# Kernel tuning notes

Measured on AMD Instinct MI355X. Metric: run time of the kernel, lower is better.

The kernel has to match this reference:

```python
import jax, jax.numpy as jnp
import numpy as np

NEG_INF = -1e9  # matches masked_fill value -1000000000.0
LEAKY_SLOPE = 0.2


def setup_inputs() -> dict:
    key = jax.random.key(0)
    k1, k2, k3, k4 = jax.random.split(key, 4)
    B, N, D_in, D_out = 8, 2048, 256, 256
    x = jax.random.normal(k1, (B, N, D_in), dtype=jnp.float32)
    adj_matrix = jax.random.randint(k2, (B, N, N), 0, 2, dtype=jnp.int32)
    # torch nn.Linear weights: W is [out, in], attention a is [1, 2*out]
    W = jax.random.normal(k3, (D_out, D_in), dtype=jnp.float32) / np.sqrt(D_in)
    a = jax.random.normal(k4, (1, 2 * D_out), dtype=jnp.float32) / np.sqrt(2 * D_out)
    return {"x": x, "adj_matrix": adj_matrix, "W": W, "a": a}


def reference(x, adj_matrix, W, a):
    # h = W(x): [B, N, D_out]
    h = jnp.einsum('bnd,od->bno', x, W)
    D = h.shape[-1]
    # attention(concat(h_i, h_j)) == h_i @ a_left + h_j @ a_right (bias-free linear)
    a_left, a_right = a[0, :D], a[0, D:]
    e = (h @ a_left)[:, :, None] + (h @ a_right)[:, None, :]  # [B, N, N]
    e = jnp.where(e > 0, e, LEAKY_SLOPE * e)  # LeakyReLU(0.2)
    e = jnp.where(adj_matrix == 0, NEG_INF, e)
    alpha = jax.nn.softmax(e, axis=-1)
    return jnp.einsum('bij,bjd->bid', alpha, h)
```

## Files before the change

### kernel.cpp

```cpp
#include <hip/hip_runtime.h>
#include <hip/hip_bf16.h>

typedef __attribute__((ext_vector_type(8))) __bf16 bf16x8;
typedef __attribute__((ext_vector_type(4))) float f32x4;
typedef __attribute__((ext_vector_type(4))) int int4v;

#define NB 8
#define NN 2048
#define ND 256
#define L2E 1.44269504f
#define AS1 __attribute__((address_space(1)))
#define AS3 __attribute__((address_space(3)))

__global__ __launch_bounds__(256) void k2_elr(
    const float* __restrict__ x, const float* __restrict__ W,
    const float* __restrict__ a, float* __restrict__ elc,
    float* __restrict__ erx) {
  __shared__ float wls[ND], wrs[ND];
  int t = threadIdx.x;
  {
    float swl = 0.f, swr = 0.f;
    for (int o = 0; o < ND; ++o) {
      float wv = W[(long)o * ND + t];
      swl = fmaf(a[o], wv, swl);
      swr = fmaf(a[ND + o], wv, swr);
    }
    wls[t] = swl;
    wrs[t] = swr;
  }
  __syncthreads();
  int r = t >> 2, q = t & 3;
  long row = (long)blockIdx.x * 64 + r;
  const f32x4* xr = (const f32x4*)(x + row * ND);
  float sl = 0.f, sr = 0.f;
#pragma unroll
  for (int ii = 0; ii < 16; ++ii) {
    int idx = q + (ii << 2);
    f32x4 xv = xr[idx];
    f32x4 lv = *(const f32x4*)(wls + idx * 4);
    f32x4 rv = *(const f32x4*)(wrs + idx * 4);
    sl += xv[0] * lv[0] + xv[1] * lv[1] + xv[2] * lv[2] + xv[3] * lv[3];
    sr += xv[0] * rv[0] + xv[1] * rv[1] + xv[2] * rv[2] + xv[3] * rv[3];
  }
  sl += __shfl_xor(sl, 1);
  sl += __shfl_xor(sl, 2);
  sr += __shfl_xor(sr, 1);
  sr += __shfl_xor(sr, 2);
  if (q == 0) {
    elc[row] = (-0.8f * sl - 16.0f) * L2E;
    erx[row] = (sr - 16.0f) * L2E;
  }
}

__global__ __launch_bounds__(256) void k1_h(
    const float* __restrict__ x, const float* __restrict__ W,
    __bf16* __restrict__ hT2) {
  __shared__ __bf16 hlds[256 * 34];
  int tid = threadIdx.x;
  int wid = tid >> 6, lane = tid & 63;
  int msub = wid & 1, nh = wid >> 1;
  int lrow = lane & 15, kg = lane >> 4;
  int m0 = blockIdx.x * 32;
  int row = m0 + msub * 16 + lrow;

  f32x4 acc[8];
#pragma unroll
  for (int f = 0; f < 8; ++f) acc[f] = (f32x4){0.f, 0.f, 0.f, 0.f};

#pragma unroll
  for (int k0 = 0; k0 < ND; k0 += 32) {
    int kk = k0 + kg * 8;
    const f32x4* xa = (const f32x4*)(x + (long)row * ND + kk);
    f32x4 a0 = xa[0], a1 = xa[1];
    bf16x8 afrag;
    afrag[0] = (__bf16)a0[0]; afrag[1] = (__bf16)a0[1];
    afrag[2] = (__bf16)a0[2]; afrag[3] = (__bf16)a0[3];
    afrag[4] = (__bf16)a1[0]; afrag[5] = (__bf16)a1[1];
    afrag[6] = (__bf16)a1[2]; afrag[7] = (__bf16)a1[3];
#pragma unroll
    for (int f = 0; f < 8; ++f) {
      int o = nh * 128 + f * 16 + lrow;
      const f32x4* wb = (const f32x4*)(W + (long)o * ND + kk);
      f32x4 b0 = wb[0], b1 = wb[1];
      bf16x8 bfrag;
      bfrag[0] = (__bf16)b0[0]; bfrag[1] = (__bf16)b0[1];
      bfrag[2] = (__bf16)b0[2]; bfrag[3] = (__bf16)b0[3];
      bfrag[4] = (__bf16)b1[0]; bfrag[5] = (__bf16)b1[1];
      bfrag[6] = (__bf16)b1[2]; bfrag[7] = (__bf16)b1[3];
      acc[f] = __builtin_amdgcn_mfma_f32_16x16x32_bf16(afrag, bfrag, acc[f], 0, 0, 0);
    }
  }

#pragma unroll
  for (int f = 0; f < 8; ++f) {
    int d = nh * 128 + f * 16 + lrow;
#pragma unroll
    for (int r = 0; r < 4; ++r) {
      int nloc = msub * 16 + kg * 4 + r;
      hlds[d * 34 + nloc] = (__bf16)acc[f][r];
    }
  }
  __syncthreads();
  {
    int b = m0 >> 11;
    int jc = (m0 & (NN - 1)) >> 5;
    const int* src = (const int*)(hlds + tid * 34);
    int tmp[16];
#pragma unroll
    for (int j = 0; j < 16; ++j) tmp[j] = src[j];
    __bf16* dst = hT2 + (((long)b * 64 + jc) * 256 + tid) * 32;
#pragma unroll
    for (int j = 0; j < 4; ++j)
      *(int4v*)(dst + j * 8) = *(int4v*)(tmp + j * 4);
  }
}

__global__ __launch_bounds__(256, 2) void k3_main(
    const int* __restrict__ adj, const __bf16* __restrict__ hT2,
    const float* __restrict__ elc, const float* __restrict__ erx,
    float* __restrict__ out) {
  __shared__ __bf16 hbuf[4][8192];
  __shared__ float er_lds[NN];
  __shared__ unsigned mask_lds[2048];

  int blk = blockIdx.x;
  int b = blk & 7;
  int it = blk >> 3;
  int tid = threadIdx.x;
  int wid = tid >> 6, lane = tid & 63;
  int lrow = lane & 15, kg = lane >> 4;
  int kg8 = kg * 8;

  const __bf16* hT2b = hT2 + (long)b * 64 * 8192;
  const int* adjb = adj + ((long)b * NN + (long)it * 32) * NN;
  const int* adjw = adjb + (long)wid * 8 * NN;
  const float* erxb = erx + (long)b * NN;

  float c1s0 = elc[b * NN + it * 32 + lrow];
  float c1s1 = elc[b * NN + it * 32 + 16 + lrow];

  __builtin_amdgcn_global_load_lds((const AS1 void*)(erxb + tid * 4),
                                   (AS3 void*)(er_lds + tid * 4), 16, 0, 0);
  __builtin_amdgcn_global_load_lds((const AS1 void*)(erxb + 1024 + tid * 4),
                                   (AS3 void*)(er_lds + 1024 + tid * 4), 16, 0, 0);

  int d0 = tid >> 2, slot = tid & 3;
  int jlog = slot ^ ((tid >> 3) & 3);
  const __bf16* sgbase = hT2b + d0 * 32 + jlog * 8;

  int hoff = (wid * 64 + lrow) * 64 + (kg ^ ((lrow >> 1) & 3)) * 16;

  f32x4 acc[2][4];
#pragma unroll
  for (int g = 0; g < 2; ++g)
#pragma unroll
    for (int f = 0; f < 4; ++f) acc[g][f] = (f32x4){0.f, 0.f, 0.f, 0.f};
  float den0 = 0.f, den1 = 0.f;

  int av0[4], av1[4];

#define STAGEH(BI, TCV)                                                       \
  {                                                                           \
    const __bf16* s_ = sgbase + (long)(TCV)*8192;                             \
    _Pragma("unroll") for (int rr = 0; rr < 4; ++rr) {                        \
      __builtin_amdgcn_global_load_lds(                                       \
          (const AS1 void*)(s_ + rr * 2048),                                  \
          (AS3 void*)(&hbuf[BI][(rr * 256 + tid) * 8]), 16, 0, 0);            \
    }                                                                         \
  }

#define ADJLOAD(S, P, H)                                                      \
  {                                                                           \
    const int* ap_ = adjw + (long)(H)*4 * NN + (long)(P)*64 + lane;           \
    _Pragma("unroll") for (int i = 0; i < 4; ++i)                             \
        av##S[i] = ap_[(long)i * NN];                                         \
  }

#define BALLOT(S, P, H)                                                       \
  {                                                                           \
    _Pragma("unroll") for (int i = 0; i < 4; ++i) {                           \
      unsigned long long mb_ = __ballot(av##S[i] != 0);                       \
      int R_ = wid * 8 + (H)*4 + i;                                           \
      if (lane == 0) {                                                        \
        mask_lds[R_ * 64 + ((2 * (P)) ^ (R_ & 31))] = (unsigned)mb_;          \
        mask_lds[R_ * 64 + ((2 * (P) + 1) ^ (R_ & 31))] = (unsigned)(mb_ >> 32); \
      }                                                                       \
    }                                                                         \
  }

#define COMPUTE(BI, TCV)                                                      \
  {                                                                           \
    unsigned msh0 = mask_lds[lrow * 64 + ((TCV) ^ lrow)] >> kg8;              \
    unsigned msh1 = mask_lds[(lrow + 16) * 64 + ((TCV) ^ lrow ^ 16)] >> kg8;  \
    const float* ep_ = er_lds + (TCV)*32 + kg8;                               \
    f32x4 x16a = *(const f32x4*)(ep_);                                        \
    f32x4 x16b = *(const f32x4*)(ep_ + 4);                                    \
    bf16x8 pf0, pf1;                                                          \
    float ps0 = 0.f, ps1 = 0.f;                                               \
    _Pragma("unroll") for (int e = 0; e < 8; ++e) {                           \
      float x16 = (e < 4) ? x16a[e] : x16b[e - 4];                            \
      float x02 = fmaf(0.2f, x16, 4.61662413f);                               \
      float m0_ = fmaxf(x16, x02 + c1s0);                                     \
      float m1_ = fmaxf(x16, x02 + c1s1);                                     \
      float p0 = __builtin_amdgcn_exp2f(m0_);                                 \
      float p1 = __builtin_amdgcn_exp2f(m1_);                                 \
      p0 = ((msh0 >> e) & 1u) ? p0 : 0.0f;                                    \
      p1 = ((msh1 >> e) & 1u) ? p1 : 0.0f;                                    \
      ps0 += p0; ps1 += p1;                                                   \
      pf0[e] = (__bf16)p0; pf1[e] = (__bf16)p1;                               \
    }                                                                         \
    den0 += ps0; den1 += ps1;                                                 \
    const char* hb_ = (const char*)&hbuf[BI][0];                              \
    __builtin_amdgcn_s_setprio(1);                                            \
    _Pragma("unroll") for (int f = 0; f < 4; ++f) {                           \
      bf16x8 bfr = *(const bf16x8*)(hb_ + hoff + f * 1024);                   \
      acc[0][f] = __builtin_amdgcn_mfma_f32_16x16x32_bf16(pf0, bfr, acc[0][f], 0, 0, 0); \
      acc[1][f] = __builtin_amdgcn_mfma_f32_16x16x32_bf16(pf1, bfr, acc[1][f], 0, 0, 0); \
    }                                                                         \
    __builtin_amdgcn_s_setprio(0);                                            \
  }

#define WAITX(VMN)                                                        \
  asm volatile("s_waitcnt vmcnt(" VMN ") lgkmcnt(0)" ::: "memory");       \
  __builtin_amdgcn_s_barrier();

  STAGEH(0, 0);
  STAGEH(1, 1);
  ADJLOAD(0, 0, 0);
  ADJLOAD(1, 0, 1);
  asm volatile("s_waitcnt vmcnt(0)" ::: "memory");
  BALLOT(0, 0, 0);
  BALLOT(1, 0, 1);
  ADJLOAD(0, 1, 0);
  ADJLOAD(1, 1, 1);
  asm volatile("s_waitcnt lgkmcnt(0)" ::: "memory");
  __builtin_amdgcn_s_barrier();

  for (int T = 0; T < 15; ++T) {
    int tc = T * 4;
    WAITX("8"); STAGEH(2, tc + 2); BALLOT(0, (tc >> 1) + 1, 0);
    ADJLOAD(0, (tc >> 1) + 2, 0); COMPUTE(0, tc);
    WAITX("8"); STAGEH(3, tc + 3); BALLOT(1, (tc >> 1) + 1, 1);
    ADJLOAD(1, (tc >> 1) + 2, 1); COMPUTE(1, tc + 1);
    WAITX("8"); STAGEH(0, tc + 4); BALLOT(0, (tc >> 1) + 2, 0);
    ADJLOAD(0, (tc >> 1) + 3, 0); COMPUTE(2, tc + 2);
    WAITX("8"); STAGEH(1, tc + 5); BALLOT(1, (tc >> 1) + 2, 1);
    ADJLOAD(1, (tc >> 1) + 3, 1); COMPUTE(3, tc + 3);
  }
  WAITX("8"); STAGEH(2, 62); BALLOT(0, 31, 0); COMPUTE(0, 60);
  WAITX("4"); STAGEH(3, 63); BALLOT(1, 31, 1); COMPUTE(1, 61);
  WAITX("4"); COMPUTE(2, 62);
  WAITX("0"); COMPUTE(3, 63);

#undef STAGEH
#undef ADJLOAD
#undef BALLOT
#undef COMPUTE
#undef WAITX

  den0 += __shfl_xor(den0, 16);
  den0 += __shfl_xor(den0, 32);
  den1 += __shfl_xor(den1, 16);
  den1 += __shfl_xor(den1, 32);
  float rdiv0[4], rdiv1[4];
#pragma unroll
  for (int r = 0; r < 4; ++r) {
    rdiv0[r] = 1.0f / __shfl(den0, kg * 4 + r);
    rdiv1[r] = 1.0f / __shfl(den1, kg * 4 + r);
  }

  float* outb = out + ((long)b * NN + (long)it * 32) * ND;
#pragma unroll
  for (int f = 0; f < 4; ++f) {
    int dcol = wid * 64 + f * 16 + lrow;
#pragma unroll
    for (int r = 0; r < 4; ++r) {
      int rr = kg * 4 + r;
      outb[(long)rr * ND + dcol] = acc[0][f][r] * rdiv0[r];
      outb[(long)(16 + rr) * ND + dcol] = acc[1][f][r] * rdiv1[r];
    }
  }
}

extern "C" void kernel_launch(void* const* d_in, const int* in_sizes, int n_in,
                              void* d_out, int out_size, void* d_ws,
                              size_t ws_size, hipStream_t stream) {
  const float* x = (const float*)d_in[0];
  const int* adj = (const int*)d_in[1];
  const float* W = (const float*)d_in[2];
  const float* a = (const float*)d_in[3];
  float* out = (float*)d_out;

  char* ws = (char*)d_ws;
  const size_t base = 8u * 1024u * 1024u;
  __bf16* hT2 = (__bf16*)ws;
  float* elc = (float*)(ws + base);
  float* erx = (float*)(ws + base + 65536u);

  k1_h<<<dim3(512), dim3(256), 0, stream>>>(x, W, hT2);
  k2_elr<<<dim3(256), dim3(256), 0, stream>>>(x, W, a, elc, erx);
  k3_main<<<dim3(512), dim3(256), 0, stream>>>(adj, hT2, elc, erx, out);
}
```

Measured before the change: 125.5 us.

## Split waves over j-halves and D-halves, read adjacency directly per lane

Re-partitions the main attention kernel so each wave owns half the key columns (alternating 32-column chunks) and half the output features, with 128-wide accumulators per wave. The ballot-based bitmask path through LDS is dropped: each lane loads its own adjacency ints as int4 vectors and uses them directly as the mask. The staged h buffer becomes double-buffered 64-key stages with a full vmcnt(0) wait each step. Partial results from the two j-halves are combined through LDS at the end. This removes ballot and LDS mask traffic but doubles accumulator registers and weakens prefetch depth.

```diff
diff --git a/kernel.cpp b/kernel.cpp
--- a/kernel.cpp
+++ b/kernel.cpp
@@ -119,23 +119,22 @@
     const int* __restrict__ adj, const __bf16* __restrict__ hT2,
     const float* __restrict__ elc, const float* __restrict__ erx,
     float* __restrict__ out) {
-  __shared__ __bf16 hbuf[4][8192];
+  __shared__ __bf16 hbuf[2][4][4096];
   __shared__ float er_lds[NN];
-  __shared__ unsigned mask_lds[2048];
+  __shared__ float denb[4][32];
 
   int blk = blockIdx.x;
   int b = blk & 7;
   int it = blk >> 3;
   int tid = threadIdx.x;
   int wid = tid >> 6, lane = tid & 63;
-  int lrow = lane & 15, kg = lane >> 4;
-  int kg8 = kg * 8;
+  int jw = wid >> 1, dw = wid & 1;
+  int lrow = lane & 15, kg = lane >> 4, kg8 = kg * 8;
 
   const __bf16* hT2b = hT2 + (long)b * 64 * 8192;
-  const int* adjb = adj + ((long)b * NN + (long)it * 32) * NN;
-  const int* adjw = adjb + (long)wid * 8 * NN;
+  const int* adjr0 = adj + ((long)b * NN + it * 32 + lrow) * NN;
+  const int* adjr1 = adjr0 + 16 * NN;
   const float* erxb = erx + (long)b * NN;
-
   float c1s0 = elc[b * NN + it * 32 + lrow];
   float c1s1 = elc[b * NN + it * 32 + 16 + lrow];
 
@@ -144,141 +143,132 @@
   __builtin_amdgcn_global_load_lds((const AS1 void*)(erxb + 1024 + tid * 4),
                                    (AS3 void*)(er_lds + 1024 + tid * 4), 16, 0, 0);
 
-  int d0 = tid >> 2, slot = tid & 3;
-  int jlog = slot ^ ((tid >> 3) & 3);
-  const __bf16* sgbase = hT2b + d0 * 32 + jlog * 8;
-
-  int hoff = (wid * 64 + lrow) * 64 + (kg ^ ((lrow >> 1) & 3)) * 16;
-
-  f32x4 acc[2][4];
-#pragma unroll
-  for (int g = 0; g < 2; ++g)
-#pragma unroll
-    for (int f = 0; f < 4; ++f) acc[g][f] = (f32x4){0.f, 0.f, 0.f, 0.f};
+  int jlog = (tid & 3) ^ ((tid >> 3) & 3);
+  int stoff = (tid >> 2) * 32 + jlog * 8;
+  int hoff = lrow * 64 + (kg ^ ((lrow >> 1) & 3)) * 16;
+
+  f32x4 acc0[8], acc1[8];
+#pragma unroll
+  for (int f = 0; f < 8; ++f) {
+    acc0[f] = (f32x4){0.f, 0.f, 0.f, 0.f};
+    acc1[f] = (f32x4){0.f, 0.f, 0.f, 0.f};
+  }
   float den0 = 0.f, den1 = 0.f;
-
-  int av0[4], av1[4];
-
-#define STAGEH(BI, TCV)                                                       \
+  int4v av0_0, av0_1, av0_2, av0_3, av1_0, av1_1, av1_2, av1_3;
+
+#define STAGE(PH, SP)                                                         \
   {                                                                           \
-    const __bf16* s_ = sgbase + (long)(TCV)*8192;                             \
-    _Pragma("unroll") for (int rr = 0; rr < 4; ++rr) {                        \
+    long cb_ = (long)(2 * (SP)) * 8192;                                       \
+    _Pragma("unroll") for (int s = 0; s < 8; ++s) {                           \
+      const __bf16* src_ = hT2b + cb_ + (s >> 2) * 8192 + ((s >> 1) & 1) * 4096 \
+                           + (s & 1) * 2048 + stoff;                          \
       __builtin_amdgcn_global_load_lds(                                       \
-          (const AS1 void*)(s_ + rr * 2048),                                  \
-          (AS3 void*)(&hbuf[BI][(rr * 256 + tid) * 8]), 16, 0, 0);            \
+          (const AS1 void*)src_,                                              \
+          (AS3 void*)(&hbuf[PH][s >> 1][(s & 1) * 2048 + tid * 8]), 16, 0, 0); \
     }                                                                         \
   }
 
-#define ADJLOAD(S, P, H)                                                      \
+#define ADJL(SET, SP)                                                         \
   {                                                                           \
-    const int* ap_ = adjw + (long)(H)*4 * NN + (long)(P)*64 + lane;           \
-    _Pragma("unroll") for (int i = 0; i < 4; ++i)                             \
-        av##S[i] = ap_[(long)i * NN];                                         \
-  }
-
-#define BALLOT(S, P, H)                                                       \
+    const int* a0_ = adjr0 + (long)(2 * (SP) + jw) * 32 + kg8;                \
+    const int* a1_ = adjr1 + (long)(2 * (SP) + jw) * 32 + kg8;                \
+    av##SET##_0 = *(const int4v*)a0_;                                         \
+    av##SET##_1 = *(const int4v*)(a0_ + 4);                                   \
+    av##SET##_2 = *(const int4v*)a1_;                                         \
+    av##SET##_3 = *(const int4v*)(a1_ + 4);                                   \
+  }
+
+#define COMP(PH, SET, SP)                                                     \
   {                                                                           \
-    _Pragma("unroll") for (int i = 0; i < 4; ++i) {                           \
-      unsigned long long mb_ = __ballot(av##S[i] != 0);                       \
-      int R_ = wid * 8 + (H)*4 + i;                                           \
-      if (lane == 0) {                                                        \
-        mask_lds[R_ * 64 + ((2 * (P)) ^ (R_ & 31))] = (unsigned)mb_;          \
-        mask_lds[R_ * 64 + ((2 * (P) + 1) ^ (R_ & 31))] = (unsigned)(mb_ >> 32); \
-      }                                                                       \
-    }                                                                         \
-  }
-
-#define COMPUTE(BI, TCV)                                                      \
-  {                                                                           \
-    unsigned msh0 = mask_lds[lrow * 64 + ((TCV) ^ lrow)] >> kg8;              \
-    unsigned msh1 = mask_lds[(lrow + 16) * 64 + ((TCV) ^ lrow ^ 16)] >> kg8;  \
-    const float* ep_ = er_lds + (TCV)*32 + kg8;                               \
-    f32x4 x16a = *(const f32x4*)(ep_);                                        \
-    f32x4 x16b = *(const f32x4*)(ep_ + 4);                                    \
+    const float* ep_ = er_lds + (2 * (SP) + jw) * 32 + kg8;                   \
+    f32x4 xa_ = *(const f32x4*)ep_;                                           \
+    f32x4 xb_ = *(const f32x4*)(ep_ + 4);                                     \
     bf16x8 pf0, pf1;                                                          \
     float ps0 = 0.f, ps1 = 0.f;                                               \
     _Pragma("unroll") for (int e = 0; e < 8; ++e) {                           \
-      float x16 = (e < 4) ? x16a[e] : x16b[e - 4];                            \
+      float x16 = (e < 4) ? xa_[e] : xb_[e - 4];                              \
       float x02 = fmaf(0.2f, x16, 4.61662413f);                               \
+      int a0v = (e < 4) ? av##SET##_0[e] : av##SET##_1[e - 4];                \
+      int a1v = (e < 4) ? av##SET##_2[e] : av##SET##_3[e - 4];                \
       float m0_ = fmaxf(x16, x02 + c1s0);                                     \
       float m1_ = fmaxf(x16, x02 + c1s1);                                     \
       float p0 = __builtin_amdgcn_exp2f(m0_);                                 \
       float p1 = __builtin_amdgcn_exp2f(m1_);                                 \
-      p0 = ((msh0 >> e) & 1u) ? p0 : 0.0f;                                    \
-      p1 = ((msh1 >> e) & 1u) ? p1 : 0.0f;                                    \
+      p0 = a0v ? p0 : 0.0f;                                                   \
+      p1 = a1v ? p1 : 0.0f;                                                   \
       ps0 += p0; ps1 += p1;                                                   \
       pf0[e] = (__bf16)p0; pf1[e] = (__bf16)p1;                               \
     }                                                                         \
     den0 += ps0; den1 += ps1;                                                 \
-    const char* hb_ = (const char*)&hbuf[BI][0];                              \
+    const char* hb_ = (const char*)&hbuf[PH][wid][0];                         \
     __builtin_amdgcn_s_setprio(1);                                            \
-    _Pragma("unroll") for (int f = 0; f < 4; ++f) {                           \
+    _Pragma("unroll") for (int f = 0; f < 8; ++f) {                           \
       bf16x8 bfr = *(const bf16x8*)(hb_ + hoff + f * 1024);                   \
-      acc[0][f] = __builtin_amdgcn_mfma_f32_16x16x32_bf16(pf0, bfr, acc[0][f], 0, 0, 0); \
-      acc[1][f] = __builtin_amdgcn_mfma_f32_16x16x32_bf16(pf1, bfr, acc[1][f], 0, 0, 0); \
+      acc0[f] = __builtin_amdgcn_mfma_f32_16x16x32_bf16(pf0, bfr, acc0[f], 0, 0, 0); \
+      acc1[f] = __builtin_amdgcn_mfma_f32_16x16x32_bf16(pf1, bfr, acc1[f], 0, 0, 0); \
     }                                                                         \
     __builtin_amdgcn_s_setprio(0);                                            \
   }
 
-#define WAITX(VMN)                                                        \
-  asm volatile("s_waitcnt vmcnt(" VMN ") lgkmcnt(0)" ::: "memory");       \
+#define WAIT0                                         \
+  asm volatile("s_waitcnt vmcnt(0)" ::: "memory");    \
   __builtin_amdgcn_s_barrier();
 
-  STAGEH(0, 0);
-  STAGEH(1, 1);
-  ADJLOAD(0, 0, 0);
-  ADJLOAD(1, 0, 1);
-  asm volatile("s_waitcnt vmcnt(0)" ::: "memory");
-  BALLOT(0, 0, 0);
-  BALLOT(1, 0, 1);
-  ADJLOAD(0, 1, 0);
-  ADJLOAD(1, 1, 1);
-  asm volatile("s_waitcnt lgkmcnt(0)" ::: "memory");
-  __builtin_amdgcn_s_barrier();
+  ADJL(0, 0);
+  STAGE(0, 0);
 
   for (int T = 0; T < 15; ++T) {
-    int tc = T * 4;
-    WAITX("8"); STAGEH(2, tc + 2); BALLOT(0, (tc >> 1) + 1, 0);
-    ADJLOAD(0, (tc >> 1) + 2, 0); COMPUTE(0, tc);
-    WAITX("8"); STAGEH(3, tc + 3); BALLOT(1, (tc >> 1) + 1, 1);
-    ADJLOAD(1, (tc >> 1) + 2, 1); COMPUTE(1, tc + 1);
-    WAITX("8"); STAGEH(0, tc + 4); BALLOT(0, (tc >> 1) + 2, 0);
-    ADJLOAD(0, (tc >> 1) + 3, 0); COMPUTE(2, tc + 2);
-    WAITX("8"); STAGEH(1, tc + 5); BALLOT(1, (tc >> 1) + 2, 1);
-    ADJLOAD(1, (tc >> 1) + 3, 1); COMPUTE(3, tc + 3);
-  }
-  WAITX("8"); STAGEH(2, 62); BALLOT(0, 31, 0); COMPUTE(0, 60);
-  WAITX("4"); STAGEH(3, 63); BALLOT(1, 31, 1); COMPUTE(1, 61);
-  WAITX("4"); COMPUTE(2, 62);
-  WAITX("0"); COMPUTE(3, 63);
-
-#undef STAGEH
-#undef ADJLOAD
-#undef BALLOT
-#undef COMPUTE
-#undef WAITX
+    int ke = 2 * T;
+    WAIT0; ADJL(1, ke + 1); STAGE(1, ke + 1); COMP(0, 0, ke);
+    WAIT0; ADJL(0, ke + 2); STAGE(0, ke + 2); COMP(1, 1, ke + 1);
+  }
+  WAIT0; ADJL(1, 31); STAGE(1, 31); COMP(0, 0, 30);
+  WAIT0; COMP(1, 1, 31);
+
+#undef STAGE
+#undef ADJL
+#undef COMP
+#undef WAIT0
 
   den0 += __shfl_xor(den0, 16);
   den0 += __shfl_xor(den0, 32);
   den1 += __shfl_xor(den1, 16);
   den1 += __shfl_xor(den1, 32);
-  float rdiv0[4], rdiv1[4];
-#pragma unroll
-  for (int r = 0; r < 4; ++r) {
-    rdiv0[r] = 1.0f / __shfl(den0, kg * 4 + r);
-    rdiv1[r] = 1.0f / __shfl(den1, kg * 4 + r);
-  }
-
-  float* outb = out + ((long)b * NN + (long)it * 32) * ND;
-#pragma unroll
-  for (int f = 0; f < 4; ++f) {
-    int dcol = wid * 64 + f * 16 + lrow;
+  if (lane < 16) {
+    denb[wid][lane] = den0;
+    denb[wid][16 + lane] = den1;
+  }
+  float* accbuf = (float*)&hbuf[0][0][0];
+  if (jw == 0) {
+#pragma unroll
+    for (int f = 0; f < 8; ++f)
+#pragma unroll
+      for (int r = 0; r < 4; ++r) {
+        accbuf[dw * 4096 + (kg * 4 + r) * 128 + f * 16 + lrow] = acc0[f][r];
+        accbuf[dw * 4096 + (16 + kg * 4 + r) * 128 + f * 16 + lrow] = acc1[f][r];
+      }
+  }
+  __syncthreads();
+  if (jw == 1) {
+    float rd0[4], rd1[4];
 #pragma unroll
     for (int r = 0; r < 4; ++r) {
-      int rr = kg * 4 + r;
-      outb[(long)rr * ND + dcol] = acc[0][f][r] * rdiv0[r];
-      outb[(long)(16 + rr) * ND + dcol] = acc[1][f][r] * rdiv1[r];
-    }
+      int r0 = kg * 4 + r;
+      rd0[r] = 1.0f / (denb[dw][r0] + denb[2 + dw][r0]);
+      rd1[r] = 1.0f / (denb[dw][16 + r0] + denb[2 + dw][16 + r0]);
+    }
+    float* ob = out + ((long)b * NN + it * 32) * ND + dw * 128;
+#pragma unroll
+    for (int f = 0; f < 8; ++f)
+#pragma unroll
+      for (int r = 0; r < 4; ++r) {
+        int r0 = kg * 4 + r;
+        int dcol = f * 16 + lrow;
+        float v0 = acc0[f][r] + accbuf[dw * 4096 + r0 * 128 + dcol];
+        float v1 = acc1[f][r] + accbuf[dw * 4096 + (16 + r0) * 128 + dcol];
+        ob[(long)r0 * ND + dcol] = v0 * rd0[r];
+        ob[(long)(16 + r0) * ND + dcol] = v1 * rd1[r];
+      }
   }
 }
 
```

Result: faster. 113.5 us (-9.6%).
